# Performance work log

Measured on AMD Instinct MI355X. Metric: run time of the kernel, lower is better.

The kernel has to match this reference:

```python
import jax, jax.numpy as jnp
import numpy as np

NUM_USER = 200000
NUM_ITEM = 100000
DIM_E = 64
N_LAYERS = 3
N_INTER = 1000000  # raw sampled interactions (deduped below)
BATCH = 8192
EDGE_DROP = 0.5    # torch uses np.random.random()*1.0; fixed here for determinism
TGT_DROP = 0.5     # self.dropout


def _xavier_uniform(key, shape):
    fan_in, fan_out = shape[0], shape[1]
    b = np.sqrt(6.0 / (fan_in + fan_out)).astype(np.float32)
    return jax.random.uniform(key, shape, jnp.float32, -b, b)


def setup_inputs() -> dict:
    rng = np.random.default_rng(0)
    u = rng.integers(0, NUM_USER, N_INTER).astype(np.int64)
    it = rng.integers(0, NUM_ITEM, N_INTER).astype(np.int64)
    pair = np.unique(u * NUM_ITEM + it)  # dedupe like the dok_matrix update
    u, it = pair // NUM_ITEM, pair % NUM_ITEM
    # symmetric bipartite adjacency A over N = U + I nodes
    rows = np.concatenate([u, it + NUM_USER])
    cols = np.concatenate([it + NUM_USER, u])
    n_nodes = NUM_USER + NUM_ITEM
    deg = np.bincount(rows, minlength=n_nodes).astype(np.float32) + 1e-7
    dinv = np.power(deg, -0.5)
    vals = (dinv[rows] * dinv[cols]).astype(np.float32)  # D^-1/2 A D^-1/2

    key = jax.random.key(0)
    k1, k2, k3, k4 = jax.random.split(key, 4)
    return {
        "user_emb": _xavier_uniform(k1, (NUM_USER, DIM_E)),
        "item_emb": _xavier_uniform(k2, (NUM_ITEM, DIM_E)),
        "adj_vals": jnp.asarray(vals),
        "adj_rows": jnp.asarray(rows),
        "adj_cols": jnp.asarray(cols),
        "users": jax.random.randint(k3, (BATCH,), 0, NUM_USER),
        "items": jax.random.randint(k4, (BATCH,), 0, NUM_ITEM),
    }


def _spmm(rows, cols, vals, x, n_nodes):
    # out[r] = sum_e vals[e] * x[cols[e]] for rows[e] == r  (COO SpMM)
    return jax.ops.segment_sum(vals[:, None] * x[cols], rows, num_segments=n_nodes)


def reference(user_emb, item_emb, adj_vals, adj_rows, adj_cols, users, items):
    n_nodes = user_emb.shape[0] + item_emb.shape[0]
    kd = jax.random.key(1234)
    ke, ku, ki = jax.random.split(kd, 3)

    # sparse edge dropout: floor(1-rate + U[0,1)) keep mask, rescale by 1/(1-rate)
    keep = jnp.floor(1.0 - EDGE_DROP + jax.random.uniform(ke, adj_vals.shape))
    vals = adj_vals * keep * (1.0 / (1.0 - EDGE_DROP))

    x = jnp.concatenate([user_emb, item_emb], axis=0)  # [N, D]
    acc = x
    for _ in range(N_LAYERS):
        x = _spmm(adj_rows, adj_cols, vals, x, n_nodes)
        acc = acc + x
    all_emb = acc / (N_LAYERS + 1)  # mean over the stacked hops

    u_all = all_emb[:user_emb.shape[0]]
    i_all = all_emb[user_emb.shape[0]:]
    u_online = u_all[users]
    i_online = i_all[items]

    # targets: detached copies with standard dropout
    u_t = jax.lax.stop_gradient(u_online)
    i_t = jax.lax.stop_gradient(i_online)
    um = jax.random.bernoulli(ku, 1.0 - TGT_DROP, u_t.shape)
    im = jax.random.bernoulli(ki, 1.0 - TGT_DROP, i_t.shape)
    u_target = jnp.where(um, u_t / (1.0 - TGT_DROP), 0.0)
    i_target = jnp.where(im, i_t / (1.0 - TGT_DROP), 0.0)
    return (u_online, u_target, i_online, i_target)
```

## Files before the change

kernel.cpp:

```cpp
#include <hip/hip_runtime.h>
#include <stdint.h>

__host__ __device__ inline void tf2x32(uint32_t k0, uint32_t k1,
                                       uint32_t x0, uint32_t x1,
                                       uint32_t& o0, uint32_t& o1) {
  const uint32_t ks2 = k0 ^ k1 ^ 0x1BD11BDAu;
  x0 += k0; x1 += k1;
#define TFR(r) { x0 += x1; x1 = (x1 << (r)) | (x1 >> (32 - (r))); x1 ^= x0; }
  TFR(13) TFR(15) TFR(26) TFR(6)
  x0 += k1;  x1 += ks2 + 1u;
  TFR(17) TFR(29) TFR(16) TFR(24)
  x0 += ks2; x1 += k0 + 2u;
  TFR(13) TFR(15) TFR(26) TFR(6)
  x0 += k0;  x1 += k1 + 3u;
  TFR(17) TFR(29) TFR(16) TFR(24)
  x0 += k1;  x1 += ks2 + 4u;
  TFR(13) TFR(15) TFR(26) TFR(6)
  x0 += ks2; x1 += k0 + 5u;
#undef TFR
  o0 = x0; o1 = x1;
}

__host__ __device__ inline uint32_t bits32(uint32_t k0, uint32_t k1, uint32_t idx) {
  uint32_t a, b;
  tf2x32(k0, k1, 0u, idx, a, b);
  return a ^ b;
}

__device__ inline bool edge_kept(uint32_t k0, uint32_t k1, uint32_t e) {
  return (bits32(k0, k1, e) >> 31) != 0u;
}

__device__ inline float bf_lo(uint32_t u) { return __uint_as_float(u << 16); }
__device__ inline float bf_hi(uint32_t u) { return __uint_as_float(u & 0xffff0000u); }
__device__ inline uint32_t bf_pack(float a, float b) {
  uint32_t lo = (__float_as_uint(a) + 0x8000u) >> 16;
  uint32_t hi = (__float_as_uint(b) + 0x8000u) & 0xffff0000u;
  return hi | lo;
}

__device__ inline void fma8_bf(float a[8], float v, const uint4& u) {
  a[0] = fmaf(v, bf_lo(u.x), a[0]); a[1] = fmaf(v, bf_hi(u.x), a[1]);
  a[2] = fmaf(v, bf_lo(u.y), a[2]); a[3] = fmaf(v, bf_hi(u.y), a[3]);
  a[4] = fmaf(v, bf_lo(u.z), a[4]); a[5] = fmaf(v, bf_hi(u.z), a[5]);
  a[6] = fmaf(v, bf_lo(u.w), a[6]); a[7] = fmaf(v, bf_hi(u.w), a[7]);
}

__global__ void k_clear(int* __restrict__ cnt, int ni,
                        uint32_t* __restrict__ f, int fwords) {
  int i = blockIdx.x * 256 + threadIdx.x;
  if (i < ni) cnt[i] = 0;
  int k = i - ni;
  if (k >= 0 && k < fwords) f[k] = 0;
}

__global__ void k_tobf16(const float* __restrict__ uemb, const float* __restrict__ iemb,
                         uint32_t* __restrict__ xe, int nu, int nn) {
  int i = blockIdx.x * 256 + threadIdx.x;
  if (i >= nn * 8) return;
  int r = i >> 3, q = i & 7;
  const float* p = (r < nu) ? uemb + (size_t)r * 64 : iemb + (size_t)(r - nu) * 64;
  float4 f0 = *(const float4*)(p + 8 * q);
  float4 f1 = *(const float4*)(p + 8 * q + 4);
  uint4 o;
  o.x = bf_pack(f0.x, f0.y); o.y = bf_pack(f0.z, f0.w);
  o.z = bf_pack(f1.x, f1.y); o.w = bf_pack(f1.z, f1.w);
  *(uint4*)(xe + (size_t)r * 32 + 4 * q) = o;
}

__global__ __launch_bounds__(1024) void k_keep(
    const int* __restrict__ rows, int E, int E2, int nu,
    unsigned long long* __restrict__ keepw, int* __restrict__ bsumE,
    int* __restrict__ cnt, uint32_t ke0, uint32_t ke1) {
  __shared__ int s[16];
  int e = blockIdx.x * 1024 + threadIdx.x;
  int lane = threadIdx.x & 63;
  int wid = threadIdx.x >> 6;
  bool kept = (e < E) && edge_kept(ke0, ke1, (uint32_t)e);
  unsigned long long m = __ballot(kept);
  int ws = blockIdx.x * 1024 + wid * 64;
  if (lane == 0 && ws < E) keepw[ws >> 6] = m;
  int nf = 0;
  if (ws + 64 <= E2) nf = __popcll(m);
  else if (ws < E2) nf = __popcll(m & ((1ull << (E2 - ws)) - 1ull));
  if (lane == 0) s[wid] = nf;
  __syncthreads();
  if (threadIdx.x == 0) {
    int t = 0;
    for (int i = 0; i < 16; ++i) t += s[i];
    bsumE[blockIdx.x] = t;
  }
  if (kept && e >= E2) atomicAdd(&cnt[rows[e] - nu], 1);
}

__device__ inline void scan_block_1024(const int* __restrict__ bsum, int nb,
                                       int* __restrict__ bpref,
                                       int* a, int* b) {
  int t = threadIdx.x;
  for (int i = t; i < 2048; i += 1024) a[i] = (i < nb) ? bsum[i] : 0;
  __syncthreads();
  int* cur = a; int* nxt = b;
  for (int off = 1; off < 2048; off <<= 1) {
    for (int i = t; i < 2048; i += 1024)
      nxt[i] = cur[i] + (i >= off ? cur[i - off] : 0);
    __syncthreads();
    int* tmp = cur; cur = nxt; nxt = tmp;
  }
  for (int i = t; i <= nb; i += 1024)
    bpref[i] = (i == 0) ? 0 : cur[i - 1];
  __syncthreads();
}

__global__ void k_scanb2x(const int* __restrict__ bA, int nA, int* __restrict__ pA,
                          const int* __restrict__ bB, int nB, int* __restrict__ pB) {
  __shared__ int a[2048], b[2048];
  scan_block_1024(bA, nA, pA, a, b);
  scan_block_1024(bB, nB, pB, a, b);
}

__global__ void k_blocksum(const int* __restrict__ cnt, int n, int* __restrict__ bsum) {
  __shared__ int s[256];
  int i = blockIdx.x * 256 + threadIdx.x;
  s[threadIdx.x] = (i < n) ? cnt[i] : 0;
  __syncthreads();
  for (int off = 128; off > 0; off >>= 1) {
    if (threadIdx.x < off) s[threadIdx.x] += s[threadIdx.x + off];
    __syncthreads();
  }
  if (threadIdx.x == 0) bsum[blockIdx.x] = s[0];
}

__global__ void k_scan_write(const int* __restrict__ cnt, int n, const int* __restrict__ bpref,
                             int* __restrict__ row_ptr, int* __restrict__ nextc) {
  __shared__ int a[256], b[256];
  int t = threadIdx.x;
  int i = blockIdx.x * 256 + t;
  int v = (i < n) ? cnt[i] : 0;
  a[t] = v;
  __syncthreads();
  int* cur = a; int* nxt = b;
  for (int off = 1; off < 256; off <<= 1) {
    nxt[t] = cur[t] + (t >= off ? cur[t - off] : 0);
    __syncthreads();
    int* tmp = cur; cur = nxt; nxt = tmp;
  }
  int incl = cur[t] + bpref[blockIdx.x];
  int excl = incl - v;
  if (i < n) { row_ptr[i] = excl; nextc[i] = excl; }
  if (i == n - 1) row_ptr[n] = incl;
}

__global__ __launch_bounds__(1024) void k_compactU(
    const int* __restrict__ rows, const int* __restrict__ cols,
    const float* __restrict__ avals, const unsigned long long* __restrict__ keepw,
    const int* __restrict__ bprefE, int E2, int nu, int nbE,
    int2* __restrict__ uslot, int* __restrict__ row_ptr_u) {
  __shared__ int a[1024], b[1024];
  int t = threadIdx.x;
  int e = blockIdx.x * 1024 + t;
  bool kept = (e < E2) && ((keepw[e >> 6] >> (e & 63)) & 1ull);
  a[t] = kept ? 1 : 0;
  __syncthreads();
  int* cur = a; int* nxt = b;
  for (int off = 1; off < 1024; off <<= 1) {
    nxt[t] = cur[t] + (t >= off ? cur[t - off] : 0);
    __syncthreads();
    int* tmp = cur; cur = nxt; nxt = tmp;
  }
  int excl = cur[t] - (kept ? 1 : 0);
  int pos = bprefE[blockIdx.x] + excl;
  if (kept) uslot[pos] = make_int2(cols[e], __float_as_int(avals[e] * 2.0f));
  if (e < E2) {
    int r = rows[e];
    int rp = (e == 0) ? -1 : rows[e - 1];
    for (int rr = rp + 1; rr <= r; ++rr) row_ptr_u[rr] = pos;
    if (e == E2 - 1) {
      int total = bprefE[nbE];
      for (int rr = r + 1; rr <= nu; ++rr) row_ptr_u[rr] = total;
    }
  }
}

__global__ void k_scatterI(const int* __restrict__ rows, const int* __restrict__ cols,
                           const float* __restrict__ avals,
                           const unsigned long long* __restrict__ keepw,
                           int E, int E2, int nu, int* __restrict__ nextc,
                           int2* __restrict__ islot) {
  int e = E2 + blockIdx.x * 256 + threadIdx.x;
  if (e >= E) return;
  if (!((keepw[e >> 6] >> (e & 63)) & 1ull)) return;
  int r = rows[e] - nu;
  int k = atomicAdd(&nextc[r], 1);
  islot[k] = make_int2(cols[e], __float_as_int(avals[e] * 2.0f));
}

__global__ void k_mark_batch(const int* __restrict__ users, const int* __restrict__ items,
                             int batch, int nu, uint8_t* fB, uint8_t* f1, uint8_t* f2) {
  int i = blockIdx.x * 256 + threadIdx.x;
  if (i >= 2 * batch) return;
  int r = (i < batch) ? users[i] : nu + items[i - batch];
  fB[r] = 1; f1[r] = 1; f2[r] = 1;
}

__global__ void k_mark_neighbors(const uint8_t* __restrict__ fin,
                                 const int* __restrict__ row_ptr_u,
                                 const int2* __restrict__ uslot,
                                 const int* __restrict__ row_ptr_i,
                                 const int2* __restrict__ islot,
                                 int n, int nu, uint8_t* __restrict__ fout) {
  int r = blockIdx.x * 256 + threadIdx.x;
  if (r >= n) return;
  if (!fin[r]) return;
  const int* rp = (r < nu) ? row_ptr_u : row_ptr_i;
  const int2* sl = (r < nu) ? uslot : islot;
  int rr = (r < nu) ? r : r - nu;
  int s = rp[rr], e = rp[rr + 1];
  for (int k = s; k < e; ++k) fout[sl[k].x] = 1;
}

__global__ void k_flagsum2(const uint8_t* __restrict__ f1, const uint8_t* __restrict__ f2,
                           int n, int* __restrict__ bsum1, int* __restrict__ bsum2) {
  __shared__ int s1[256], s2[256];
  int i = blockIdx.x * 256 + threadIdx.x;
  s1[threadIdx.x] = (i < n) ? (int)f1[i] : 0;
  s2[threadIdx.x] = (i < n) ? (int)f2[i] : 0;
  __syncthreads();
  for (int off = 128; off > 0; off >>= 1) {
    if (threadIdx.x < off) {
      s1[threadIdx.x] += s1[threadIdx.x + off];
      s2[threadIdx.x] += s2[threadIdx.x + off];
    }
    __syncthreads();
  }
  if (threadIdx.x == 0) { bsum1[blockIdx.x] = s1[0]; bsum2[blockIdx.x] = s2[0]; }
}

__global__ void k_compact2(const uint8_t* __restrict__ f1, const uint8_t* __restrict__ f2,
                           int n, const int* __restrict__ bpref1,
                           const int* __restrict__ bpref2,
                           int* __restrict__ list1, int* __restrict__ list2) {
  __shared__ int a[256], b[256];
  int t = threadIdx.x;
  int i = blockIdx.x * 256 + t;

  int v = (i < n) ? (int)f1[i] : 0;
  a[t] = v;
  __syncthreads();
  int* cur = a; int* nxt = b;
  for (int off = 1; off < 256; off <<= 1) {
    nxt[t] = cur[t] + (t >= off ? cur[t - off] : 0);
    __syncthreads();
    int* tmp = cur; cur = nxt; nxt = tmp;
  }
  if (v) list1[bpref1[blockIdx.x] + cur[t] - 1] = i;
  __syncthreads();

  v = (i < n) ? (int)f2[i] : 0;
  a[t] = v;
  __syncthreads();
  cur = a; nxt = b;
  for (int off = 1; off < 256; off <<= 1) {
    nxt[t] = cur[t] + (t >= off ? cur[t - off] : 0);
    __syncthreads();
    int* tmp = cur; cur = nxt; nxt = tmp;
  }
  if (v) list2[bpref2[blockIdx.x] + cur[t] - 1] = i;
}

__global__ __launch_bounds__(256) void k_spmm(
    const int* __restrict__ row_ptr_u, const int2* __restrict__ uslot,
    const int* __restrict__ row_ptr_i, const int2* __restrict__ islot,
    const uint32_t* __restrict__ xin, uint32_t* __restrict__ xout,
    const int* __restrict__ rowlist, const int* __restrict__ nrows_p, int nu) {
  int nrows = *nrows_p;
  int i = blockIdx.x * 32 + (threadIdx.x >> 3);
  if (i >= nrows) return;
  int r = rowlist[i];
  int j = threadIdx.x & 7;
  bool isu = r < nu;
  const int* rp = isu ? row_ptr_u : row_ptr_i;
  const int2* sl = isu ? uslot : islot;
  int rr = isu ? r : r - nu;
  int s = rp[rr], e = rp[rr + 1];
  float a[8] = {0, 0, 0, 0, 0, 0, 0, 0};
  int last = e - 1;
  for (int k = s; k < e; k += 4) {
    int i1 = (k + 1 <= last) ? k + 1 : last;
    int i2 = (k + 2 <= last) ? k + 2 : last;
    int i3 = (k + 3 <= last) ? k + 3 : last;
    int2 s0 = sl[k], s1 = sl[i1], s2 = sl[i2], s3 = sl[i3];
    float v0 = __int_as_float(s0.y);
    float v1 = (k + 1 <= last) ? __int_as_float(s1.y) : 0.0f;
    float v2 = (k + 2 <= last) ? __int_as_float(s2.y) : 0.0f;
    float v3 = (k + 3 <= last) ? __int_as_float(s3.y) : 0.0f;
    uint4 u0 = *(const uint4*)(xin + (size_t)s0.x * 32 + 4 * j);
    uint4 u1 = *(const uint4*)(xin + (size_t)s1.x * 32 + 4 * j);
    uint4 u2 = *(const uint4*)(xin + (size_t)s2.x * 32 + 4 * j);
    uint4 u3 = *(const uint4*)(xin + (size_t)s3.x * 32 + 4 * j);
    fma8_bf(a, v0, u0);
    fma8_bf(a, v1, u1);
    fma8_bf(a, v2, u2);
    fma8_bf(a, v3, u3);
  }
  uint4 o;
  o.x = bf_pack(a[0], a[1]); o.y = bf_pack(a[2], a[3]);
  o.z = bf_pack(a[4], a[5]); o.w = bf_pack(a[6], a[7]);
  *(uint4*)(xout + (size_t)r * 32 + 4 * j) = o;
}

__global__ void k_gatherA(const uint32_t* __restrict__ x0, const float* __restrict__ uemb,
                          const float* __restrict__ iemb, const int* __restrict__ users,
                          const int* __restrict__ items, float* __restrict__ out,
                          int batch, int nu) {
  int b = blockIdx.x * 32 + (threadIdx.x >> 3);
  if (b >= 2 * batch) return;
  int j = threadIdx.x & 7;
  size_t H = (size_t)batch * 64;
  int row; size_t dst; bool isu = b < batch;
  if (isu) {
    row = users[b];
    dst = (size_t)b * 64 + 8 * j;
  } else {
    int bi = b - batch;
    row = items[bi];
    dst = 2 * H + (size_t)bi * 64 + 8 * j;
  }
  const float* p = (isu ? uemb + (size_t)row * 64 : iemb + (size_t)row * 64) + 8 * j;
  float4 t0 = *(const float4*)p;
  float4 t1 = *(const float4*)(p + 4);
  int xr = isu ? row : nu + row;
  uint4 u = *(const uint4*)(x0 + (size_t)xr * 32 + 4 * j);
  t0.x += bf_lo(u.x); t0.y += bf_hi(u.x); t0.z += bf_lo(u.y); t0.w += bf_hi(u.y);
  t1.x += bf_lo(u.z); t1.y += bf_hi(u.z); t1.z += bf_lo(u.w); t1.w += bf_hi(u.w);
  *(float4*)(out + dst) = t0;
  *(float4*)(out + dst + 4) = t1;
}

__global__ __launch_bounds__(256) void k_tail(
    const int* __restrict__ row_ptr_u, const int2* __restrict__ uslot,
    const int* __restrict__ row_ptr_i, const int2* __restrict__ islot,
    const uint32_t* __restrict__ x1, const int* __restrict__ users,
    const int* __restrict__ items, float* __restrict__ out,
    int batch, int nu,
    uint32_t ku0, uint32_t ku1, uint32_t ki0, uint32_t ki1) {
  int b = blockIdx.x * 32 + (threadIdx.x >> 3);
  if (b >= 2 * batch) return;
  int j = threadIdx.x & 7;
  size_t H = (size_t)batch * 64;
  const int* rp; const int2* sl; int rr; size_t dst; int f0; uint32_t mk0, mk1;
  bool isu = b < batch;
  if (isu) {
    rr = users[b];
    rp = row_ptr_u; sl = uslot;
    dst = (size_t)b * 64 + 8 * j;
    f0 = b * 64 + 8 * j;
    mk0 = ku0; mk1 = ku1;
  } else {
    int bi = b - batch;
    rr = items[bi];
    rp = row_ptr_i; sl = islot;
    dst = 2 * H + (size_t)bi * 64 + 8 * j;
    f0 = bi * 64 + 8 * j;
    mk0 = ki0; mk1 = ki1;
  }
  int s = rp[rr], e = rp[rr + 1];
  float a[8] = {0, 0, 0, 0, 0, 0, 0, 0};
  int last = e - 1;
  for (int k = s; k < e; k += 4) {
    int i1 = (k + 1 <= last) ? k + 1 : last;
    int i2 = (k + 2 <= last) ? k + 2 : last;
    int i3 = (k + 3 <= last) ? k + 3 : last;
    int2 s0 = sl[k], s1 = sl[i1], s2 = sl[i2], s3 = sl[i3];
    float v0 = __int_as_float(s0.y);
    float v1 = (k + 1 <= last) ? __int_as_float(s1.y) : 0.0f;
    float v2 = (k + 2 <= last) ? __int_as_float(s2.y) : 0.0f;
    float v3 = (k + 3 <= last) ? __int_as_float(s3.y) : 0.0f;
    uint4 u0 = *(const uint4*)(x1 + (size_t)s0.x * 32 + 4 * j);
    uint4 u1 = *(const uint4*)(x1 + (size_t)s1.x * 32 + 4 * j);
    uint4 u2 = *(const uint4*)(x1 + (size_t)s2.x * 32 + 4 * j);
    uint4 u3 = *(const uint4*)(x1 + (size_t)s3.x * 32 + 4 * j);
    fma8_bf(a, v0, u0);
    fma8_bf(a, v1, u1);
    fma8_bf(a, v2, u2);
    fma8_bf(a, v3, u3);
  }
  int xr = isu ? rr : nu + rr;
  uint4 u = *(const uint4*)(x1 + (size_t)xr * 32 + 4 * j);
  float* o = out + dst;
  float4 t0 = *(float4*)o;
  float4 t1 = *(float4*)(o + 4);
  t0.x += bf_lo(u.x); t0.y += bf_hi(u.x); t0.z += bf_lo(u.y); t0.w += bf_hi(u.y);
  t1.x += bf_lo(u.z); t1.y += bf_hi(u.z); t1.z += bf_lo(u.w); t1.w += bf_hi(u.w);
  t0.x += a[0]; t0.y += a[1]; t0.z += a[2]; t0.w += a[3];
  t1.x += a[4]; t1.y += a[5]; t1.z += a[6]; t1.w += a[7];
  float ov[8] = {t0.x * 0.25f, t0.y * 0.25f, t0.z * 0.25f, t0.w * 0.25f,
                 t1.x * 0.25f, t1.y * 0.25f, t1.z * 0.25f, t1.w * 0.25f};
  float tv[8];
#pragma unroll
  for (int c = 0; c < 8; ++c) {
    bool present = (bits32(mk0, mk1, (uint32_t)(f0 + c)) >> 31) == 0u;
    tv[c] = present ? ov[c] * 2.0f : 0.0f;
  }
  *(float4*)o = make_float4(ov[0], ov[1], ov[2], ov[3]);
  *(float4*)(o + 4) = make_float4(ov[4], ov[5], ov[6], ov[7]);
  *(float4*)(o + H) = make_float4(tv[0], tv[1], tv[2], tv[3]);
  *(float4*)(o + H + 4) = make_float4(tv[4], tv[5], tv[6], tv[7]);
}

extern "C" void kernel_launch(void* const* d_in, const int* in_sizes, int n_in,
                              void* d_out, int out_size, void* d_ws, size_t ws_size,
                              hipStream_t stream) {
  const float* uemb  = (const float*)d_in[0];
  const float* iemb  = (const float*)d_in[1];
  const float* avals = (const float*)d_in[2];
  const int*   rows  = (const int*)d_in[3];
  const int*   cols  = (const int*)d_in[4];
  const int*   users = (const int*)d_in[5];
  const int*   items = (const int*)d_in[6];
  const int DIM = 64;
  const int NU = in_sizes[0] / DIM;
  const int NI = in_sizes[1] / DIM;
  const int E  = in_sizes[2];
  const int E2 = E / 2;
  const int B = in_sizes[5];
  const int NN = NU + NI;
  float* out = (float*)d_out;
  (void)n_in; (void)out_size; (void)ws_size;

  uint32_t ke0, ke1, ku0, ku1, ki0, ki1;
  tf2x32(0u, 1234u, 0u, 0u, ke0, ke1);
  tf2x32(0u, 1234u, 0u, 1u, ku0, ku1);
  tf2x32(0u, 1234u, 0u, 2u, ki0, ki1);

  char* p = (char*)d_ws;
  auto carve = [&](size_t bytes) {
    char* r = p;
    p += (bytes + 255) & ~(size_t)255;
    return (void*)r;
  };
  uint32_t* Xe    = (uint32_t*)carve((size_t)NN * 32 * 4);
  uint32_t* X0    = (uint32_t*)carve((size_t)NN * 32 * 4);
  uint32_t* X1    = (uint32_t*)carve((size_t)NN * 32 * 4);
  int2*  uslot    = (int2*)carve((size_t)E2 * 8);
  int2*  islot    = (int2*)carve((size_t)(E - E2) * 8);
  unsigned long long* keepw = (unsigned long long*)carve(((size_t)E / 64 + 2) * 8);
  int*   cnt      = (int*)carve((size_t)NI * 4);
  int*   row_ptr_u = (int*)carve((size_t)(NU + 1) * 4);
  int*   row_ptr_i = (int*)carve((size_t)(NI + 1) * 4);
  int*   nextc    = (int*)carve((size_t)NI * 4);
  uint8_t* fB     = (uint8_t*)carve((size_t)NN * 3);
  uint8_t* f1     = fB + NN;
  uint8_t* f2     = fB + 2 * (size_t)NN;
  int*   list1    = (int*)carve((size_t)NN * 4);
  int*   list2    = (int*)carve((size_t)NN * 4);
  const int GK    = (E + 1023) / 1024;
  const int NBE   = (E2 + 1023) / 1024;
  const int NBI   = (NI + 255) / 256;
  const int NB    = (NN + 255) / 256;
  int*   bsumE    = (int*)carve((size_t)GK * 4);
  int*   bprefE   = (int*)carve((size_t)(NBE + 1) * 4);
  int*   bsumI    = (int*)carve((size_t)NBI * 4);
  int*   bprefI   = (int*)carve((size_t)(NBI + 1) * 4);
  int*   bsum1    = (int*)carve((size_t)NB * 4);
  int*   bpref1   = (int*)carve((size_t)(NB + 1) * 4);
  int*   bsum2    = (int*)carve((size_t)NB * 4);
  int*   bpref2   = (int*)carve((size_t)(NB + 1) * 4);

  {
    const int fwords = (int)(((size_t)NN * 3 + 3) / 4);
    const int gC = (NI + fwords + 255) / 256;
    k_clear<<<gC, 256, 0, stream>>>(cnt, NI, (uint32_t*)fB, fwords);
  }
  k_tobf16<<<(NN * 8 + 255) / 256, 256, 0, stream>>>(uemb, iemb, Xe, NU, NN);

  k_keep<<<GK, 1024, 0, stream>>>(rows, E, E2, NU, keepw, bsumE, cnt, ke0, ke1);
  k_blocksum<<<NBI, 256, 0, stream>>>(cnt, NI, bsumI);
  k_scanb2x<<<1, 1024, 0, stream>>>(bsumE, NBE, bprefE, bsumI, NBI, bprefI);
  k_scan_write<<<NBI, 256, 0, stream>>>(cnt, NI, bprefI, row_ptr_i, nextc);
  k_compactU<<<NBE, 1024, 0, stream>>>(rows, cols, avals, keepw, bprefE, E2, NU, NBE,
                                       uslot, row_ptr_u);
  {
    const int gI = (E - E2 + 255) / 256;
    k_scatterI<<<gI, 256, 0, stream>>>(rows, cols, avals, keepw, E, E2, NU, nextc, islot);
  }

  const int gB = (2 * B + 255) / 256;
  const int gN = (NN + 255) / 256;
  k_mark_batch<<<gB, 256, 0, stream>>>(users, items, B, NU, fB, f1, f2);
  k_mark_neighbors<<<gN, 256, 0, stream>>>(fB, row_ptr_u, uslot, row_ptr_i, islot, NN, NU, f2);
  k_mark_neighbors<<<gN, 256, 0, stream>>>(f2, row_ptr_u, uslot, row_ptr_i, islot, NN, NU, f1);
  k_flagsum2<<<NB, 256, 0, stream>>>(f1, f2, NN, bsum1, bsum2);
  k_scanb2x<<<1, 1024, 0, stream>>>(bsum1, NB, bpref1, bsum2, NB, bpref2);
  k_compact2<<<NB, 256, 0, stream>>>(f1, f2, NN, bpref1, bpref2, list1, list2);

  const int gG = (2 * B + 31) / 32;
  const int gS = (NN + 31) / 32;

  k_spmm<<<gS, 256, 0, stream>>>(row_ptr_u, uslot, row_ptr_i, islot, Xe, X0,
                                 list1, bpref1 + NB, NU);
  k_gatherA<<<gG, 256, 0, stream>>>(X0, uemb, iemb, users, items, out, B, NU);
  k_spmm<<<gS, 256, 0, stream>>>(row_ptr_u, uslot, row_ptr_i, islot, X0, X1,
                                 list2, bpref2 + NB, NU);
  k_tail<<<gG, 256, 0, stream>>>(row_ptr_u, uslot, row_ptr_i, islot, X1,
                                 users, items, out, B, NU, ku0, ku1, ki0, ki1);
}
```

Before: 166.0 us.

## Run first SpMM hop densely and drop second frontier pass and kernels

The first propagation hop now runs over all nodes through a new dense k_spmm_all kernel, so the second neighbor-marking pass and the list1 compaction are gone. The clear and bf16 conversion kernels are merged into one init kernel, batch marking moves into k_keep, and the gatherA work is folded into k_tail. This removes several kernel launches and a frontier pass. In exchange, hop one now does SpMM over every row instead of only the 2-hop frontier, which adds memory traffic.

```diff
diff --git a/kernel.cpp b/kernel.cpp
--- a/kernel.cpp
+++ b/kernel.cpp
@@ -46,17 +46,15 @@
   a[6] = fmaf(v, bf_lo(u.w), a[6]); a[7] = fmaf(v, bf_hi(u.w), a[7]);
 }
 
-__global__ void k_clear(int* __restrict__ cnt, int ni,
-                        uint32_t* __restrict__ f, int fwords) {
+__global__ void k_init(int* __restrict__ cnt, int ni,
+                       uint32_t* __restrict__ flagw, int fw,
+                       const float* __restrict__ uemb, const float* __restrict__ iemb,
+                       uint32_t* __restrict__ xe, int nu, int nn) {
   int i = blockIdx.x * 256 + threadIdx.x;
-  if (i < ni) cnt[i] = 0;
-  int k = i - ni;
-  if (k >= 0 && k < fwords) f[k] = 0;
-}
-
-__global__ void k_tobf16(const float* __restrict__ uemb, const float* __restrict__ iemb,
-                         uint32_t* __restrict__ xe, int nu, int nn) {
-  int i = blockIdx.x * 256 + threadIdx.x;
+  if (i < ni) { cnt[i] = 0; return; }
+  i -= ni;
+  if (i < fw) { flagw[i] = 0; return; }
+  i -= fw;
   if (i >= nn * 8) return;
   int r = i >> 3, q = i & 7;
   const float* p = (r < nu) ? uemb + (size_t)r * 64 : iemb + (size_t)(r - nu) * 64;
@@ -71,7 +69,10 @@
 __global__ __launch_bounds__(1024) void k_keep(
     const int* __restrict__ rows, int E, int E2, int nu,
     unsigned long long* __restrict__ keepw, int* __restrict__ bsumE,
-    int* __restrict__ cnt, uint32_t ke0, uint32_t ke1) {
+    int* __restrict__ cnt, const int* __restrict__ users,
+    const int* __restrict__ items, int batch,
+    uint8_t* __restrict__ fB, uint8_t* __restrict__ f2,
+    uint32_t ke0, uint32_t ke1) {
   __shared__ int s[16];
   int e = blockIdx.x * 1024 + threadIdx.x;
   int lane = threadIdx.x & 63;
@@ -91,6 +92,10 @@
     bsumE[blockIdx.x] = t;
   }
   if (kept && e >= E2) atomicAdd(&cnt[rows[e] - nu], 1);
+  if (e < 2 * batch) {
+    int r = (e < batch) ? users[e] : nu + items[e - batch];
+    fB[r] = 1; f2[r] = 1;
+  }
 }
 
 __device__ inline void scan_block_1024(const int* __restrict__ bsum, int nb,
@@ -116,6 +121,11 @@
   __shared__ int a[2048], b[2048];
   scan_block_1024(bA, nA, pA, a, b);
   scan_block_1024(bB, nB, pB, a, b);
+}
+
+__global__ void k_scanb1(const int* __restrict__ bA, int nA, int* __restrict__ pA) {
+  __shared__ int a[2048], b[2048];
+  scan_block_1024(bA, nA, pA, a, b);
 }
 
 __global__ void k_blocksum(const int* __restrict__ cnt, int n, int* __restrict__ bsum) {
@@ -192,14 +202,6 @@
   int r = rows[e] - nu;
   int k = atomicAdd(&nextc[r], 1);
   islot[k] = make_int2(cols[e], __float_as_int(avals[e] * 2.0f));
-}
-
-__global__ void k_mark_batch(const int* __restrict__ users, const int* __restrict__ items,
-                             int batch, int nu, uint8_t* fB, uint8_t* f1, uint8_t* f2) {
-  int i = blockIdx.x * 256 + threadIdx.x;
-  if (i >= 2 * batch) return;
-  int r = (i < batch) ? users[i] : nu + items[i - batch];
-  fB[r] = 1; f1[r] = 1; f2[r] = 1;
 }
 
 __global__ void k_mark_neighbors(const uint8_t* __restrict__ fin,
@@ -218,32 +220,24 @@
   for (int k = s; k < e; ++k) fout[sl[k].x] = 1;
 }
 
-__global__ void k_flagsum2(const uint8_t* __restrict__ f1, const uint8_t* __restrict__ f2,
-                           int n, int* __restrict__ bsum1, int* __restrict__ bsum2) {
-  __shared__ int s1[256], s2[256];
+__global__ void k_flagsum1(const uint8_t* __restrict__ f, int n, int* __restrict__ bsum) {
+  __shared__ int s1[256];
   int i = blockIdx.x * 256 + threadIdx.x;
-  s1[threadIdx.x] = (i < n) ? (int)f1[i] : 0;
-  s2[threadIdx.x] = (i < n) ? (int)f2[i] : 0;
+  s1[threadIdx.x] = (i < n) ? (int)f[i] : 0;
   __syncthreads();
   for (int off = 128; off > 0; off >>= 1) {
-    if (threadIdx.x < off) {
-      s1[threadIdx.x] += s1[threadIdx.x + off];
-      s2[threadIdx.x] += s2[threadIdx.x + off];
-    }
-    __syncthreads();
-  }
-  if (threadIdx.x == 0) { bsum1[blockIdx.x] = s1[0]; bsum2[blockIdx.x] = s2[0]; }
-}
-
-__global__ void k_compact2(const uint8_t* __restrict__ f1, const uint8_t* __restrict__ f2,
-                           int n, const int* __restrict__ bpref1,
-                           const int* __restrict__ bpref2,
-                           int* __restrict__ list1, int* __restrict__ list2) {
+    if (threadIdx.x < off) s1[threadIdx.x] += s1[threadIdx.x + off];
+    __syncthreads();
+  }
+  if (threadIdx.x == 0) bsum[blockIdx.x] = s1[0];
+}
+
+__global__ void k_compact1(const uint8_t* __restrict__ f, int n,
+                           const int* __restrict__ bpref, int* __restrict__ list) {
   __shared__ int a[256], b[256];
   int t = threadIdx.x;
   int i = blockIdx.x * 256 + t;
-
-  int v = (i < n) ? (int)f1[i] : 0;
+  int v = (i < n) ? (int)f[i] : 0;
   a[t] = v;
   __syncthreads();
   int* cur = a; int* nxt = b;
@@ -252,19 +246,46 @@
     __syncthreads();
     int* tmp = cur; cur = nxt; nxt = tmp;
   }
-  if (v) list1[bpref1[blockIdx.x] + cur[t] - 1] = i;
-  __syncthreads();
-
-  v = (i < n) ? (int)f2[i] : 0;
-  a[t] = v;
-  __syncthreads();
-  cur = a; nxt = b;
-  for (int off = 1; off < 256; off <<= 1) {
-    nxt[t] = cur[t] + (t >= off ? cur[t - off] : 0);
-    __syncthreads();
-    int* tmp = cur; cur = nxt; nxt = tmp;
-  }
-  if (v) list2[bpref2[blockIdx.x] + cur[t] - 1] = i;
+  if (v) list[bpref[blockIdx.x] + cur[t] - 1] = i;
+}
+
+__global__ __launch_bounds__(256) void k_spmm_all(
+    const int* __restrict__ row_ptr_u, const int2* __restrict__ uslot,
+    const int* __restrict__ row_ptr_i, const int2* __restrict__ islot,
+    const uint32_t* __restrict__ xin, uint32_t* __restrict__ xout,
+    int nn, int nu) {
+  int r = blockIdx.x * 32 + (threadIdx.x >> 3);
+  if (r >= nn) return;
+  int j = threadIdx.x & 7;
+  bool isu = r < nu;
+  const int* rp = isu ? row_ptr_u : row_ptr_i;
+  const int2* sl = isu ? uslot : islot;
+  int rr = isu ? r : r - nu;
+  int s = rp[rr], e = rp[rr + 1];
+  float a[8] = {0, 0, 0, 0, 0, 0, 0, 0};
+  int last = e - 1;
+  for (int k = s; k < e; k += 4) {
+    int i1 = (k + 1 <= last) ? k + 1 : last;
+    int i2 = (k + 2 <= last) ? k + 2 : last;
+    int i3 = (k + 3 <= last) ? k + 3 : last;
+    int2 s0 = sl[k], s1 = sl[i1], s2 = sl[i2], s3 = sl[i3];
+    float v0 = __int_as_float(s0.y);
+    float v1 = (k + 1 <= last) ? __int_as_float(s1.y) : 0.0f;
+    float v2 = (k + 2 <= last) ? __int_as_float(s2.y) : 0.0f;
+    float v3 = (k + 3 <= last) ? __int_as_float(s3.y) : 0.0f;
+    uint4 u0 = *(const uint4*)(xin + (size_t)s0.x * 32 + 4 * j);
+    uint4 u1 = *(const uint4*)(xin + (size_t)s1.x * 32 + 4 * j);
+    uint4 u2 = *(const uint4*)(xin + (size_t)s2.x * 32 + 4 * j);
+    uint4 u3 = *(const uint4*)(xin + (size_t)s3.x * 32 + 4 * j);
+    fma8_bf(a, v0, u0);
+    fma8_bf(a, v1, u1);
+    fma8_bf(a, v2, u2);
+    fma8_bf(a, v3, u3);
+  }
+  uint4 o;
+  o.x = bf_pack(a[0], a[1]); o.y = bf_pack(a[2], a[3]);
+  o.z = bf_pack(a[4], a[5]); o.w = bf_pack(a[6], a[7]);
+  *(uint4*)(xout + (size_t)r * 32 + 4 * j) = o;
 }
 
 __global__ __launch_bounds__(256) void k_spmm(
@@ -308,40 +329,13 @@
   *(uint4*)(xout + (size_t)r * 32 + 4 * j) = o;
 }
 
-__global__ void k_gatherA(const uint32_t* __restrict__ x0, const float* __restrict__ uemb,
-                          const float* __restrict__ iemb, const int* __restrict__ users,
-                          const int* __restrict__ items, float* __restrict__ out,
-                          int batch, int nu) {
-  int b = blockIdx.x * 32 + (threadIdx.x >> 3);
-  if (b >= 2 * batch) return;
-  int j = threadIdx.x & 7;
-  size_t H = (size_t)batch * 64;
-  int row; size_t dst; bool isu = b < batch;
-  if (isu) {
-    row = users[b];
-    dst = (size_t)b * 64 + 8 * j;
-  } else {
-    int bi = b - batch;
-    row = items[bi];
-    dst = 2 * H + (size_t)bi * 64 + 8 * j;
-  }
-  const float* p = (isu ? uemb + (size_t)row * 64 : iemb + (size_t)row * 64) + 8 * j;
-  float4 t0 = *(const float4*)p;
-  float4 t1 = *(const float4*)(p + 4);
-  int xr = isu ? row : nu + row;
-  uint4 u = *(const uint4*)(x0 + (size_t)xr * 32 + 4 * j);
-  t0.x += bf_lo(u.x); t0.y += bf_hi(u.x); t0.z += bf_lo(u.y); t0.w += bf_hi(u.y);
-  t1.x += bf_lo(u.z); t1.y += bf_hi(u.z); t1.z += bf_lo(u.w); t1.w += bf_hi(u.w);
-  *(float4*)(out + dst) = t0;
-  *(float4*)(out + dst + 4) = t1;
-}
-
 __global__ __launch_bounds__(256) void k_tail(
     const int* __restrict__ row_ptr_u, const int2* __restrict__ uslot,
     const int* __restrict__ row_ptr_i, const int2* __restrict__ islot,
-    const uint32_t* __restrict__ x1, const int* __restrict__ users,
-    const int* __restrict__ items, float* __restrict__ out,
-    int batch, int nu,
+    const uint32_t* __restrict__ x0, const uint32_t* __restrict__ x1,
+    const float* __restrict__ uemb, const float* __restrict__ iemb,
+    const int* __restrict__ users, const int* __restrict__ items,
+    float* __restrict__ out, int batch, int nu,
     uint32_t ku0, uint32_t ku1, uint32_t ki0, uint32_t ki1) {
   int b = blockIdx.x * 32 + (threadIdx.x >> 3);
   if (b >= 2 * batch) return;
@@ -384,13 +378,16 @@
     fma8_bf(a, v2, u2);
     fma8_bf(a, v3, u3);
   }
+  const float* pe = (isu ? uemb + (size_t)rr * 64 : iemb + (size_t)rr * 64) + 8 * j;
+  float4 t0 = *(const float4*)pe;
+  float4 t1 = *(const float4*)(pe + 4);
   int xr = isu ? rr : nu + rr;
-  uint4 u = *(const uint4*)(x1 + (size_t)xr * 32 + 4 * j);
-  float* o = out + dst;
-  float4 t0 = *(float4*)o;
-  float4 t1 = *(float4*)(o + 4);
-  t0.x += bf_lo(u.x); t0.y += bf_hi(u.x); t0.z += bf_lo(u.y); t0.w += bf_hi(u.y);
-  t1.x += bf_lo(u.z); t1.y += bf_hi(u.z); t1.z += bf_lo(u.w); t1.w += bf_hi(u.w);
+  uint4 u0r = *(const uint4*)(x0 + (size_t)xr * 32 + 4 * j);
+  t0.x += bf_lo(u0r.x); t0.y += bf_hi(u0r.x); t0.z += bf_lo(u0r.y); t0.w += bf_hi(u0r.y);
+  t1.x += bf_lo(u0r.z); t1.y += bf_hi(u0r.z); t1.z += bf_lo(u0r.w); t1.w += bf_hi(u0r.w);
+  uint4 u1r = *(const uint4*)(x1 + (size_t)xr * 32 + 4 * j);
+  t0.x += bf_lo(u1r.x); t0.y += bf_hi(u1r.x); t0.z += bf_lo(u1r.y); t0.w += bf_hi(u1r.y);
+  t1.x += bf_lo(u1r.z); t1.y += bf_hi(u1r.z); t1.z += bf_lo(u1r.w); t1.w += bf_hi(u1r.w);
   t0.x += a[0]; t0.y += a[1]; t0.z += a[2]; t0.w += a[3];
   t1.x += a[4]; t1.y += a[5]; t1.z += a[6]; t1.w += a[7];
   float ov[8] = {t0.x * 0.25f, t0.y * 0.25f, t0.z * 0.25f, t0.w * 0.25f,
@@ -401,6 +398,7 @@
     bool present = (bits32(mk0, mk1, (uint32_t)(f0 + c)) >> 31) == 0u;
     tv[c] = present ? ov[c] * 2.0f : 0.0f;
   }
+  float* o = out + dst;
   *(float4*)o = make_float4(ov[0], ov[1], ov[2], ov[3]);
   *(float4*)(o + 4) = make_float4(ov[4], ov[5], ov[6], ov[7]);
   *(float4*)(o + H) = make_float4(tv[0], tv[1], tv[2], tv[3]);
@@ -448,10 +446,8 @@
   int*   row_ptr_u = (int*)carve((size_t)(NU + 1) * 4);
   int*   row_ptr_i = (int*)carve((size_t)(NI + 1) * 4);
   int*   nextc    = (int*)carve((size_t)NI * 4);
-  uint8_t* fB     = (uint8_t*)carve((size_t)NN * 3);
-  uint8_t* f1     = fB + NN;
-  uint8_t* f2     = fB + 2 * (size_t)NN;
-  int*   list1    = (int*)carve((size_t)NN * 4);
+  uint8_t* fB     = (uint8_t*)carve((size_t)NN * 2);
+  uint8_t* f2     = fB + NN;
   int*   list2    = (int*)carve((size_t)NN * 4);
   const int GK    = (E + 1023) / 1024;
   const int NBE   = (E2 + 1023) / 1024;
@@ -461,19 +457,17 @@
   int*   bprefE   = (int*)carve((size_t)(NBE + 1) * 4);
   int*   bsumI    = (int*)carve((size_t)NBI * 4);
   int*   bprefI   = (int*)carve((size_t)(NBI + 1) * 4);
-  int*   bsum1    = (int*)carve((size_t)NB * 4);
-  int*   bpref1   = (int*)carve((size_t)(NB + 1) * 4);
   int*   bsum2    = (int*)carve((size_t)NB * 4);
   int*   bpref2   = (int*)carve((size_t)(NB + 1) * 4);
 
   {
-    const int fwords = (int)(((size_t)NN * 3 + 3) / 4);
-    const int gC = (NI + fwords + 255) / 256;
-    k_clear<<<gC, 256, 0, stream>>>(cnt, NI, (uint32_t*)fB, fwords);
-  }
-  k_tobf16<<<(NN * 8 + 255) / 256, 256, 0, stream>>>(uemb, iemb, Xe, NU, NN);
-
-  k_keep<<<GK, 1024, 0, stream>>>(rows, E, E2, NU, keepw, bsumE, cnt, ke0, ke1);
+    const int fw = (int)(((size_t)NN * 2 + 3) / 4);
+    const int gI = (NI + fw + NN * 8 + 255) / 256;
+    k_init<<<gI, 256, 0, stream>>>(cnt, NI, (uint32_t*)fB, fw, uemb, iemb, Xe, NU, NN);
+  }
+
+  k_keep<<<GK, 1024, 0, stream>>>(rows, E, E2, NU, keepw, bsumE, cnt,
+                                  users, items, B, fB, f2, ke0, ke1);
   k_blocksum<<<NBI, 256, 0, stream>>>(cnt, NI, bsumI);
   k_scanb2x<<<1, 1024, 0, stream>>>(bsumE, NBE, bprefE, bsumI, NBI, bprefI);
   k_scan_write<<<NBI, 256, 0, stream>>>(cnt, NI, bprefI, row_ptr_i, nextc);
@@ -484,23 +478,19 @@
     k_scatterI<<<gI, 256, 0, stream>>>(rows, cols, avals, keepw, E, E2, NU, nextc, islot);
   }
 
-  const int gB = (2 * B + 255) / 256;
   const int gN = (NN + 255) / 256;
-  k_mark_batch<<<gB, 256, 0, stream>>>(users, items, B, NU, fB, f1, f2);
   k_mark_neighbors<<<gN, 256, 0, stream>>>(fB, row_ptr_u, uslot, row_ptr_i, islot, NN, NU, f2);
-  k_mark_neighbors<<<gN, 256, 0, stream>>>(f2, row_ptr_u, uslot, row_ptr_i, islot, NN, NU, f1);
-  k_flagsum2<<<NB, 256, 0, stream>>>(f1, f2, NN, bsum1, bsum2);
-  k_scanb2x<<<1, 1024, 0, stream>>>(bsum1, NB, bpref1, bsum2, NB, bpref2);
-  k_compact2<<<NB, 256, 0, stream>>>(f1, f2, NN, bpref1, bpref2, list1, list2);
+  k_flagsum1<<<NB, 256, 0, stream>>>(f2, NN, bsum2);
+  k_scanb1<<<1, 1024, 0, stream>>>(bsum2, NB, bpref2);
+  k_compact1<<<NB, 256, 0, stream>>>(f2, NN, bpref2, list2);
 
   const int gG = (2 * B + 31) / 32;
   const int gS = (NN + 31) / 32;
 
-  k_spmm<<<gS, 256, 0, stream>>>(row_ptr_u, uslot, row_ptr_i, islot, Xe, X0,
-                                 list1, bpref1 + NB, NU);
-  k_gatherA<<<gG, 256, 0, stream>>>(X0, uemb, iemb, users, items, out, B, NU);
+  k_spmm_all<<<gS, 256, 0, stream>>>(row_ptr_u, uslot, row_ptr_i, islot, Xe, X0, NN, NU);
   k_spmm<<<gS, 256, 0, stream>>>(row_ptr_u, uslot, row_ptr_i, islot, X0, X1,
                                  list2, bpref2 + NB, NU);
-  k_tail<<<gG, 256, 0, stream>>>(row_ptr_u, uslot, row_ptr_i, islot, X1,
-                                 users, items, out, B, NU, ku0, ku1, ki0, ki1);
-}
+  k_tail<<<gG, 256, 0, stream>>>(row_ptr_u, uslot, row_ptr_i, islot, X0, X1,
+                                 uemb, iemb, users, items, out, B, NU,
+                                 ku0, ku1, ki0, ki1);
+}
```

After: 156.4 us, median of 2. 5.8% less time.
